# Performance work log

Measured on AMD Instinct MI355X. Metric: run time of the kernel, lower is better.

The kernel has to match this reference:

```python
import jax, jax.numpy as jnp
import numpy as np

FP16_MIN = -65504.0
FP16_MAX = 65504.0

B, S, D, H = 2, 2048, 1024, 16
HD = D // H


def setup_inputs() -> dict:
    key = jax.random.key(0)
    ks = jax.random.split(key, 12)
    s = 0.02
    inp = {
        "x_q": jax.random.normal(ks[0], (B, S, D), jnp.float32),
        "x_k": jax.random.normal(ks[1], (B, S, D), jnp.float32),
        "x_v": jax.random.normal(ks[2], (B, S, D), jnp.float32),
        # causal mask [B, 1, S, S]; 0 entries are masked out
        "mask": jnp.broadcast_to(jnp.tril(jnp.ones((S, S), jnp.int32)), (B, 1, S, S)),
        "Wq": jax.random.normal(ks[3], (D, D), jnp.float32) * s,
        "bq": jnp.zeros((D,), jnp.float32),
        "Wk": jax.random.normal(ks[4], (D, D), jnp.float32) * s,
        "bk": jnp.zeros((D,), jnp.float32),
        "Wv": jax.random.normal(ks[5], (D, D), jnp.float32) * s,
        "bv": jnp.zeros((D,), jnp.float32),
        "Wo": jax.random.normal(ks[6], (D, D), jnp.float32) * s,
        "bo": jnp.zeros((D,), jnp.float32),
    }
    return inp


def _split_heads(x):
    # [B, S, D] -> [B, H, S, HD]
    b, s, _ = x.shape
    return x.reshape(b, s, H, HD).transpose(0, 2, 1, 3)


def reference(x_q, x_k, x_v, mask, Wq, bq, Wk, bk, Wv, bv, Wo, bo):
    scale = jnp.sqrt(jnp.float32(HD))
    q = _split_heads(x_q @ Wq + bq)  # [B,H,S,HD]
    k = _split_heads(x_k @ Wk + bk)
    v = _split_heads(x_v @ Wv + bv)

    scores = jnp.einsum("bhqd,bhkd->bhqk", q, k) / scale  # [B,H,S,S]
    scores = jnp.where(mask == 0, FP16_MIN, scores)
    scores = jnp.where(jnp.isneginf(scores), FP16_MIN, scores)
    scores = jnp.where(jnp.isposinf(scores), FP16_MAX, scores)

    probs = jax.nn.softmax(scores, axis=-1)  # dropout p=0.0 -> identity
    ctx = jnp.einsum("bhqk,bhkd->bhqd", probs, v)  # [B,H,S,HD]
    ctx = ctx.transpose(0, 2, 1, 3).reshape(x_q.shape[0], x_q.shape[1], D)
    out = ctx @ Wo + bo
    return out, probs
```

## Files before the change

### kernel.cpp

```cpp
#include <hip/hip_runtime.h>


typedef __bf16 bf16x8 __attribute__((ext_vector_type(8)));
typedef float f32x4 __attribute__((ext_vector_type(4)));

__device__ __forceinline__ unsigned short f2bf(float f) {
  unsigned int u = __builtin_bit_cast(unsigned int, f);
  u += 0x7fffu + ((u >> 16) & 1u);
  return (unsigned short)(u >> 16);
}
__device__ __forceinline__ float bf2f_lo(unsigned int u) {
  return __builtin_bit_cast(float, u << 16);
}
__device__ __forceinline__ float bf2f_hi(unsigned int u) {
  return __builtin_bit_cast(float, u & 0xffff0000u);
}

__global__ void transpose_w(const float* __restrict__ W0, const float* __restrict__ W1,
                            const float* __restrict__ W2, const float* __restrict__ W3,
                            unsigned short* __restrict__ Wt) {
  __shared__ float t[32][33];
  const int z = blockIdx.z;
  const float* W = (z == 0) ? W0 : (z == 1) ? W1 : (z == 2) ? W2 : W3;
  unsigned short* o = Wt + (size_t)z * 1048576u;
  const int n0 = blockIdx.x * 32, k0 = blockIdx.y * 32;
  const int tx = threadIdx.x, ty = threadIdx.y;
#pragma unroll
  for (int i = 0; i < 4; i++)
    t[ty + 8 * i][tx] = W[(size_t)(k0 + ty + 8 * i) * 1024 + n0 + tx];
  __syncthreads();
#pragma unroll
  for (int i = 0; i < 4; i++)
    o[(size_t)(n0 + ty + 8 * i) * 1024 + k0 + tx] = f2bf(t[tx][ty + 8 * i]);
}

__global__ __launch_bounds__(256) void gemm_kernel(
    const void* __restrict__ A0, const void* __restrict__ A1, const void* __restrict__ A2,
    const unsigned short* __restrict__ Wtb,
    const float* __restrict__ b0, const float* __restrict__ b1, const float* __restrict__ b2,
    void* __restrict__ O0, void* __restrict__ O1, void* __restrict__ O2,
    const int mode0) {
  __shared__ unsigned short Alds[64 * 72];
  const int z = blockIdx.z;
  const int mode = mode0 + z;
  const void* Av = (z == 0) ? A0 : (z == 1) ? A1 : A2;
  const float* bias = (z == 0) ? b0 : (z == 1) ? b1 : b2;
  void* outv = (z == 0) ? O0 : (z == 1) ? O1 : O2;
  const unsigned short* Wt = Wtb + (size_t)z * 1048576u;

  const int tid = threadIdx.x;
  const int lane = tid & 63;
  const int wave = tid >> 6;
  const int wm = wave >> 1, wn = wave & 1;
  const int m0 = blockIdx.y * 64, n0 = blockIdx.x * 128;
  const int g = lane >> 4, c = lane & 15;

  f32x4 acc[2][4];
#pragma unroll
  for (int i = 0; i < 2; i++)
#pragma unroll
    for (int j = 0; j < 4; j++) acc[i][j] = (f32x4){0.f, 0.f, 0.f, 0.f};

  const int srow = tid >> 2;
  const int sch = (tid & 3) * 16;

  uint4 pk0, pk1;
#define LOAD_PACK(KB)                                                             \
  if (mode < 3) {                                                                 \
    const float* A = (const float*)Av;                                            \
    const float4* src = (const float4*)(A + (size_t)(m0 + srow) * 1024 + (KB) + sch); \
    const float4 v0 = src[0], v1 = src[1], v2 = src[2], v3 = src[3];              \
    pk0.x = (unsigned int)f2bf(v0.x) | ((unsigned int)f2bf(v0.y) << 16);          \
    pk0.y = (unsigned int)f2bf(v0.z) | ((unsigned int)f2bf(v0.w) << 16);          \
    pk0.z = (unsigned int)f2bf(v1.x) | ((unsigned int)f2bf(v1.y) << 16);          \
    pk0.w = (unsigned int)f2bf(v1.z) | ((unsigned int)f2bf(v1.w) << 16);          \
    pk1.x = (unsigned int)f2bf(v2.x) | ((unsigned int)f2bf(v2.y) << 16);          \
    pk1.y = (unsigned int)f2bf(v2.z) | ((unsigned int)f2bf(v2.w) << 16);          \
    pk1.z = (unsigned int)f2bf(v3.x) | ((unsigned int)f2bf(v3.y) << 16);          \
    pk1.w = (unsigned int)f2bf(v3.z) | ((unsigned int)f2bf(v3.w) << 16);          \
  } else {                                                                        \
    const unsigned short* A = (const unsigned short*)Av;                          \
    const uint4* src = (const uint4*)(A + (size_t)(m0 + srow) * 1024 + (KB) + sch); \
    pk0 = src[0];                                                                 \
    pk1 = src[1];                                                                 \
  }

  LOAD_PACK(0);
  for (int kb = 0; kb < 1024; kb += 64) {
    *(uint4*)&Alds[srow * 72 + sch] = pk0;
    *(uint4*)&Alds[srow * 72 + sch + 8] = pk1;
    if (kb + 64 < 1024) { LOAD_PACK(kb + 64); }
    __syncthreads();

    bf16x8 af[2][2], bfr[4][2];
#pragma unroll
    for (int mi = 0; mi < 2; mi++)
#pragma unroll
      for (int kk = 0; kk < 2; kk++)
        af[mi][kk] = *(const bf16x8*)&Alds[(wm * 32 + mi * 16 + c) * 72 + kk * 32 + g * 8];
#pragma unroll
    for (int nf = 0; nf < 4; nf++)
#pragma unroll
      for (int kk = 0; kk < 2; kk++)
        bfr[nf][kk] = *(const bf16x8*)(Wt + (size_t)(n0 + wn * 64 + nf * 16 + c) * 1024 + kb + kk * 32 + g * 8);
#pragma unroll
    for (int kk = 0; kk < 2; kk++)
#pragma unroll
      for (int mi = 0; mi < 2; mi++)
#pragma unroll
        for (int nf = 0; nf < 4; nf++)
          acc[mi][nf] = __builtin_amdgcn_mfma_f32_16x16x32_bf16(af[mi][kk], bfr[nf][kk], acc[mi][nf], 0, 0, 0);
    __syncthreads();
  }
#undef LOAD_PACK

#pragma unroll
  for (int nf = 0; nf < 4; nf++) {
    const int col = n0 + wn * 64 + nf * 16 + c;
    const float bc = bias[col];
#pragma unroll
    for (int mi = 0; mi < 2; mi++) {
#pragma unroll
      for (int r = 0; r < 4; r++) {
        const int row = m0 + wm * 32 + mi * 16 + g * 4 + r;
        const float v = acc[mi][nf][r] + bc;
        if (mode == 0) {
          ((unsigned short*)outv)[(size_t)row * 1024 + col] = f2bf(v * 0.125f);
        } else if (mode == 1) {
          ((unsigned short*)outv)[(size_t)row * 1024 + col] = f2bf(v);
        } else if (mode == 2) {
          const int bb = row >> 11, s = row & 2047;
          ((unsigned short*)outv)[((size_t)(bb * 1024 + col)) * 2048 + s] = f2bf(v);
        } else {
          ((float*)outv)[(size_t)row * 1024 + col] = v;
        }
      }
    }
  }
}

__global__ __launch_bounds__(512, 4) void attn_kernel(
    const unsigned short* __restrict__ Q, const unsigned short* __restrict__ K,
    const unsigned short* __restrict__ Vt, float* __restrict__ probs,
    unsigned short* __restrict__ ctx) {
  __shared__ unsigned short Klds[64 * 72];
  __shared__ unsigned short Vlds[64 * 72];
  __shared__ unsigned short Plds[128 * 72];

  const int tid = threadIdx.x;
  const int lane = tid & 63, wave = tid >> 6;
  const int g = lane >> 4, c = lane & 15;
  const int bh = blockIdx.x;
  const int b = bh >> 4, h = bh & 15;
  const int q0 = blockIdx.y * 128;
  const int qrow0 = q0 + wave * 16;
  const int wave_kend = qrow0 + 16;

  const unsigned short* Qh = Q + ((size_t)(b * 2048 + qrow0)) * 1024 + h * 64;
  const unsigned short* Kh = K + ((size_t)b * 2048) * 1024 + h * 64;
  const unsigned short* Vh = Vt + ((size_t)bh) * 64 * 2048;
  float* Ph = probs + ((size_t)(bh * 2048 + q0)) * 2048;

  const bf16x8 qa0 = *(const bf16x8*)&Qh[(size_t)c * 1024 + g * 8];
  const bf16x8 qa1 = *(const bf16x8*)&Qh[(size_t)c * 1024 + 32 + g * 8];

  const int srow = tid >> 3;
  const int scol = (tid & 7) * 8;
  const int kb_end = q0 + 128;

  float lp[4] = {0.f, 0.f, 0.f, 0.f};
  f32x4 cacc[4];
#pragma unroll
  for (int nf = 0; nf < 4; nf++) cacc[nf] = (f32x4){0.f, 0.f, 0.f, 0.f};

  uint4 kreg = *(const uint4*)(Kh + (size_t)srow * 1024 + scol);
  uint4 vreg = *(const uint4*)(Vh + (size_t)srow * 2048 + scol);
  for (int kb = 0; kb < kb_end; kb += 64) {
    *(uint4*)&Klds[srow * 72 + scol] = kreg;
    *(uint4*)&Vlds[srow * 72 + scol] = vreg;
    if (kb + 64 < kb_end) {
      kreg = *(const uint4*)(Kh + (size_t)(kb + 64 + srow) * 1024 + scol);
      vreg = *(const uint4*)(Vh + (size_t)srow * 2048 + kb + 64 + scol);
    }
    __syncthreads();

    if (kb < wave_kend) {
      f32x4 sv[4];
#pragma unroll
      for (int sub = 0; sub < 4; sub++) {
        sv[sub] = (f32x4){0.f, 0.f, 0.f, 0.f};
        const unsigned short* Kr = &Klds[(sub * 16 + c) * 72];
        sv[sub] = __builtin_amdgcn_mfma_f32_16x16x32_bf16(qa0, *(const bf16x8*)&Kr[g * 8], sv[sub], 0, 0, 0);
        sv[sub] = __builtin_amdgcn_mfma_f32_16x16x32_bf16(qa1, *(const bf16x8*)&Kr[32 + g * 8], sv[sub], 0, 0, 0);
      }
      if (kb + 63 > qrow0) {
#pragma unroll
        for (int sub = 0; sub < 4; sub++)
#pragma unroll
          for (int r = 0; r < 4; r++)
            if (kb + sub * 16 + c > qrow0 + g * 4 + r) sv[sub][r] = -1e30f;
      }
#pragma unroll
      for (int sub = 0; sub < 4; sub++)
#pragma unroll
        for (int r = 0; r < 4; r++) {
          const float pu = __expf(sv[sub][r]);
          lp[r] += pu;
          Plds[(wave * 16 + g * 4 + r) * 72 + sub * 16 + c] = f2bf(pu);
        }
      const bf16x8 pa0 = *(const bf16x8*)&Plds[(wave * 16 + c) * 72 + g * 8];
      const bf16x8 pa1 = *(const bf16x8*)&Plds[(wave * 16 + c) * 72 + 32 + g * 8];
#pragma unroll
      for (int nf = 0; nf < 4; nf++) {
        const bf16x8 vf0 = *(const bf16x8*)&Vlds[(nf * 16 + c) * 72 + g * 8];
        const bf16x8 vf1 = *(const bf16x8*)&Vlds[(nf * 16 + c) * 72 + 32 + g * 8];
        cacc[nf] = __builtin_amdgcn_mfma_f32_16x16x32_bf16(pa0, vf0, cacc[nf], 0, 0, 0);
        cacc[nf] = __builtin_amdgcn_mfma_f32_16x16x32_bf16(pa1, vf1, cacc[nf], 0, 0, 0);
      }
    }
    __syncthreads();

    {
      const int prow = tid >> 2;
      const int pcb = (tid & 3) * 16;
      unsigned short* dst = (unsigned short*)Ph + (size_t)prow * 4096 + kb + pcb;
      const int rw_kend = q0 + (prow & ~15) + 16;
      if (kb < rw_kend) {
        *(uint4*)dst = *(const uint4*)&Plds[prow * 72 + pcb];
        *(uint4*)(dst + 8) = *(const uint4*)&Plds[prow * 72 + pcb + 8];
      } else {
        *(uint4*)dst = make_uint4(0u, 0u, 0u, 0u);
        *(uint4*)(dst + 8) = make_uint4(0u, 0u, 0u, 0u);
      }
    }
  }

#pragma unroll
  for (int off = 1; off < 16; off <<= 1)
#pragma unroll
    for (int r = 0; r < 4; r++) lp[r] += __shfl_xor(lp[r], off);
  float invl[4];
#pragma unroll
  for (int r = 0; r < 4; r++) invl[r] = 1.0f / lp[r];

#pragma unroll
  for (int nf = 0; nf < 4; nf++)
#pragma unroll
    for (int r = 0; r < 4; r++)
      ctx[((size_t)(b * 2048 + qrow0 + g * 4 + r)) * 1024 + h * 64 + nf * 16 + c] =
          f2bf(cacc[nf][r] * invl[r]);
}

__global__ __launch_bounds__(256) void norm_probs(float* __restrict__ probs) {
  const int wv = (blockIdx.x * 256 + threadIdx.x) >> 6;
  const int lane = threadIdx.x & 63;
  for (int row = wv; row < 65536; row += 8192) {
    const int q = row & 2047;
    const int kbe = ((q >> 7) + 1) << 7;
    float* base = probs + (size_t)row * 2048;
    const unsigned short* srcb = (const unsigned short*)base;

    uint2 rw[8];
#pragma unroll
    for (int i = 0; i < 8; i++) {
      const int col = i * 256 + lane * 4;
      if (col < kbe) rw[i] = *(const uint2*)(srcb + col);
      else rw[i] = make_uint2(0u, 0u);
    }
    float f[32];
#pragma unroll
    for (int i = 0; i < 8; i++) {
      f[i * 4 + 0] = bf2f_lo(rw[i].x);
      f[i * 4 + 1] = bf2f_hi(rw[i].x);
      f[i * 4 + 2] = bf2f_lo(rw[i].y);
      f[i * 4 + 3] = bf2f_hi(rw[i].y);
    }
    float s = 0.f;
#pragma unroll
    for (int i = 0; i < 32; i++) s += f[i];
#pragma unroll
    for (int off = 1; off < 64; off <<= 1) s += __shfl_xor(s, off);
    const float il = 1.0f / s;
#pragma unroll
    for (int i = 0; i < 8; i++)
      *(float4*)(base + i * 256 + lane * 4) =
          make_float4(f[i * 4 + 0] * il, f[i * 4 + 1] * il,
                      f[i * 4 + 2] * il, f[i * 4 + 3] * il);
  }
}

extern "C" void kernel_launch(void* const* d_in, const int* in_sizes, int n_in,
                              void* d_out, int out_size, void* d_ws, size_t ws_size,
                              hipStream_t stream) {
  if (ws_size < (size_t)40 * 1024 * 1024) return;

  const float* xq = (const float*)d_in[0];
  const float* xk = (const float*)d_in[1];
  const float* xv = (const float*)d_in[2];
  const float* Wq = (const float*)d_in[4];
  const float* bq = (const float*)d_in[5];
  const float* Wk = (const float*)d_in[6];
  const float* bk = (const float*)d_in[7];
  const float* Wv = (const float*)d_in[8];
  const float* bv = (const float*)d_in[9];
  const float* Wo = (const float*)d_in[10];
  const float* bo = (const float*)d_in[11];

  unsigned short* ws = (unsigned short*)d_ws;
  unsigned short* Wt = ws;
  unsigned short* Qw = ws + (size_t)4 * 1048576u;
  unsigned short* Kw = Qw + 4194304u;
  unsigned short* Vtw = Kw + 4194304u;
  unsigned short* Cw = Vtw + 4194304u;

  float* out = (float*)d_out;
  float* probs = out + 4194304u;

  transpose_w<<<dim3(32, 32, 4), dim3(32, 8), 0, stream>>>(Wq, Wk, Wv, Wo, Wt);
  gemm_kernel<<<dim3(8, 64, 3), 256, 0, stream>>>(xq, xk, xv, Wt, bq, bk, bv,
                                                  Qw, Kw, Vtw, 0);
  attn_kernel<<<dim3(32, 16, 1), 512, 0, stream>>>(Qw, Kw, Vtw, probs, Cw);
  norm_probs<<<dim3(2048), 256, 0, stream>>>(probs);
  gemm_kernel<<<dim3(8, 64, 1), 256, 0, stream>>>(Cw, Cw, Cw, Wt + 3u * 1048576u,
                                                  bo, bo, bo, out, out, out, 3);
}
```

Measured before the change: 373.9 us.

## Fuse probability normalization into attention kernel epilogue

Removes the separate norm_probs launch. Each attention wave now normalizes its own 16 probability rows at the end, reading back the bf16 unnormalized values it wrote and rewriting them as fp32. It reuses the row sums it already computed, so the reread and reduction pass disappear. The zero-fill of masked tiles is also dropped from the main loop because the epilogue writes zeros beyond the valid range. The risk is a longer tail in the attention kernel, and the in-place bf16-to-fp32 expansion relies on visibility of the wave's own global writes and on row ordering.

```diff
diff --git a/kernel.cpp b/kernel.cpp
--- a/kernel.cpp
+++ b/kernel.cpp
@@ -223,14 +223,11 @@
     {
       const int prow = tid >> 2;
       const int pcb = (tid & 3) * 16;
-      unsigned short* dst = (unsigned short*)Ph + (size_t)prow * 4096 + kb + pcb;
       const int rw_kend = q0 + (prow & ~15) + 16;
       if (kb < rw_kend) {
+        unsigned short* dst = (unsigned short*)Ph + (size_t)prow * 4096 + kb + pcb;
         *(uint4*)dst = *(const uint4*)&Plds[prow * 72 + pcb];
         *(uint4*)(dst + 8) = *(const uint4*)&Plds[prow * 72 + pcb + 8];
-      } else {
-        *(uint4*)dst = make_uint4(0u, 0u, 0u, 0u);
-        *(uint4*)(dst + 8) = make_uint4(0u, 0u, 0u, 0u);
       }
     }
   }
@@ -249,43 +246,32 @@
     for (int r = 0; r < 4; r++)
       ctx[((size_t)(b * 2048 + qrow0 + g * 4 + r)) * 1024 + h * 64 + nf * 16 + c] =
           f2bf(cacc[nf][r] * invl[r]);
-}
-
-__global__ __launch_bounds__(256) void norm_probs(float* __restrict__ probs) {
-  const int wv = (blockIdx.x * 256 + threadIdx.x) >> 6;
-  const int lane = threadIdx.x & 63;
-  for (int row = wv; row < 65536; row += 8192) {
-    const int q = row & 2047;
-    const int kbe = ((q >> 7) + 1) << 7;
-    float* base = probs + (size_t)row * 2048;
-    const unsigned short* srcb = (const unsigned short*)base;
-
+
+  float rs[16];
+#pragma unroll
+  for (int rr = 0; rr < 16; rr++)
+    rs[rr] = __shfl(lp[rr & 3], (rr >> 2) << 4);
+  asm volatile("s_waitcnt vmcnt(0)" ::: "memory");
+
+  const int ve = wave_kend;
+#pragma unroll 1
+  for (int rr = 0; rr < 16; rr++) {
+    const float il = 1.0f / rs[rr];
+    const unsigned short* srcb = (const unsigned short*)Ph + (size_t)(wave * 16 + rr) * 4096;
+    float* dstr = Ph + (size_t)(wave * 16 + rr) * 2048;
     uint2 rw[8];
 #pragma unroll
     for (int i = 0; i < 8; i++) {
       const int col = i * 256 + lane * 4;
-      if (col < kbe) rw[i] = *(const uint2*)(srcb + col);
+      if (col < ve) rw[i] = *(const uint2*)(srcb + col);
       else rw[i] = make_uint2(0u, 0u);
     }
-    float f[32];
 #pragma unroll
     for (int i = 0; i < 8; i++) {
-      f[i * 4 + 0] = bf2f_lo(rw[i].x);
-      f[i * 4 + 1] = bf2f_hi(rw[i].x);
-      f[i * 4 + 2] = bf2f_lo(rw[i].y);
-      f[i * 4 + 3] = bf2f_hi(rw[i].y);
-    }
-    float s = 0.f;
-#pragma unroll
-    for (int i = 0; i < 32; i++) s += f[i];
-#pragma unroll
-    for (int off = 1; off < 64; off <<= 1) s += __shfl_xor(s, off);
-    const float il = 1.0f / s;
-#pragma unroll
-    for (int i = 0; i < 8; i++)
-      *(float4*)(base + i * 256 + lane * 4) =
-          make_float4(f[i * 4 + 0] * il, f[i * 4 + 1] * il,
-                      f[i * 4 + 2] * il, f[i * 4 + 3] * il);
+      const int col = i * 256 + lane * 4;
+      *(float4*)(dstr + col) = make_float4(bf2f_lo(rw[i].x) * il, bf2f_hi(rw[i].x) * il,
+                                           bf2f_lo(rw[i].y) * il, bf2f_hi(rw[i].y) * il);
+    }
   }
 }
 
@@ -320,7 +306,6 @@
   gemm_kernel<<<dim3(8, 64, 3), 256, 0, stream>>>(xq, xk, xv, Wt, bq, bk, bv,
                                                   Qw, Kw, Vtw, 0);
   attn_kernel<<<dim3(32, 16, 1), 512, 0, stream>>>(Qw, Kw, Vtw, probs, Cw);
-  norm_probs<<<dim3(2048), 256, 0, stream>>>(probs);
   gemm_kernel<<<dim3(8, 64, 1), 256, 0, stream>>>(Cw, Cw, Cw, Wt + 3u * 1048576u,
                                                   bo, bo, bo, out, out, out, 3);
 }
```

New measurement: 391.1 us. 1.05x slower.
